# Optimization experiments

Hardware: AMD Instinct MI355X
Metric: run time of the kernel (lower is better)

## Reference

```python
import jax, jax.numpy as jnp
import numpy as np

NUM_HEADS = 16


def setup_inputs() -> dict:
    key = jax.random.key(0)
    k1, k2, k3, k4 = jax.random.split(key, 4)
    B, N, C = 4, 2048, 1024
    x = jax.random.normal(k1, (B, N, C), dtype=jnp.float32)
    # xavier-uniform-ish scaling for stable softmax
    Wqkv = jax.random.normal(k2, (C, 3 * C), dtype=jnp.float32) * (2.0 / (C + 3 * C)) ** 0.5
    Wproj = jax.random.normal(k3, (C, C), dtype=jnp.float32) * (1.0 / C) ** 0.5
    bproj = jnp.zeros((C,), dtype=jnp.float32)
    mask = jax.random.randint(k4, (B, N), 0, 2, dtype=jnp.int32)  # >0 means masked
    return {"x": x, "Wqkv": Wqkv, "Wproj": Wproj, "bproj": bproj, "mask": mask}


def reference(x, Wqkv, Wproj, bproj, mask):
    B, N, C = x.shape
    H = NUM_HEADS
    Dh = C // H
    scale = Dh ** -0.5
    qkv = x @ Wqkv                                   # [B, N, 3C]
    qkv = qkv.reshape(B, N, 3, H, Dh).transpose(2, 0, 3, 1, 4)  # [3, B, H, N, Dh]
    q, k, v = qkv[0], qkv[1], qkv[2]
    att = jnp.einsum('bhqd,bhkd->bhqk', q, k) * scale  # [B, H, N, N]
    att = jnp.where(mask[:, None, None, :] > 0, jnp.float32(-10000000.0), att)
    att = jax.nn.softmax(att, axis=-1)
    out = jnp.einsum('bhqk,bhkd->bhqd', att, v)      # [B, H, N, Dh]
    out = out.transpose(0, 2, 1, 3).reshape(B, N, C)
    return out @ Wproj + bproj
```

## Files before the change

kernel.cpp:

```cpp
#include <hip/hip_runtime.h>
#include <hip/hip_bf16.h>
#include <cstdint>

typedef __bf16 bf16x8 __attribute__((ext_vector_type(8)));
typedef float f32x4 __attribute__((ext_vector_type(4)));
typedef uint4 __attribute__((may_alias)) uint4a;

typedef __attribute__((address_space(3))) unsigned int   lds_u32;
typedef __attribute__((address_space(1))) const unsigned int gbl_u32;

#define BATCH 4
#define SEQ   2048
#define CDIM  1024
#define NH    16
#define HD    64
#define MROWS (BATCH*SEQ)

__device__ __forceinline__ unsigned short f2bf(float f) {
    uint32_t u = __builtin_bit_cast(uint32_t, f);
    u += 0x7fffu + ((u >> 16) & 1u);
    return (unsigned short)(u >> 16);
}

__device__ __forceinline__ void g2l16(const unsigned short* g, unsigned short* l) {
    __builtin_amdgcn_global_load_lds((gbl_u32*)g, (lds_u32*)l, 16, 0, 0);
}

__global__ void cvt_bf16_kernel(const float* __restrict__ in,
                                unsigned short* __restrict__ out, int n) {
    int i = (blockIdx.x * blockDim.x + threadIdx.x) * 4;
    if (i + 3 < n) {
        float4 v = *(const float4*)(in + i);
        ushort4 o;
        o.x = f2bf(v.x); o.y = f2bf(v.y); o.z = f2bf(v.z); o.w = f2bf(v.w);
        *(ushort4*)(out + i) = o;
    }
}

__global__ void transpose_cvt_kernel(const float* __restrict__ in,
                                     unsigned short* __restrict__ out,
                                     int R, int Cc) {
    __shared__ float tile[32][33];
    int c0 = blockIdx.x * 32, r0 = blockIdx.y * 32;
    int tx = threadIdx.x, ty = threadIdx.y;
    #pragma unroll
    for (int i = 0; i < 32; i += 8)
        tile[ty + i][tx] = in[(size_t)(r0 + ty + i) * Cc + c0 + tx];
    __syncthreads();
    #pragma unroll
    for (int i = 0; i < 32; i += 8)
        out[(size_t)(c0 + ty + i) * R + r0 + tx] = f2bf(tile[tx][ty + i]);
}

__global__ void mask_scan_kernel(const int* __restrict__ mask,
                                 int* __restrict__ pfx, int* __restrict__ cnt) {
    __shared__ int s[256];
    int b = blockIdx.x, t = threadIdx.x;
    int keep[8], lc = 0;
    #pragma unroll
    for (int u = 0; u < 8; ++u) {
        keep[u] = (mask[b * SEQ + t * 8 + u] > 0) ? 0 : 1;
        lc += keep[u];
    }
    s[t] = lc;
    __syncthreads();
    for (int d = 1; d < 256; d <<= 1) {
        int w = (t >= d) ? s[t - d] : 0;
        __syncthreads();
        s[t] += w;
        __syncthreads();
    }
    int pos = s[t] - lc;
    #pragma unroll
    for (int u = 0; u < 8; ++u) {
        int idx = b * SEQ + t * 8 + u;
        pfx[idx] = keep[u] ? pos++ : -1;
    }
    if (t == 255) cnt[b] = s[255];
}

#define BK 64

__global__ __launch_bounds__(256, 2)
void gemm_qkv_kernel(const unsigned short* __restrict__ A,
                     const unsigned short* __restrict__ Bt,
                     const int* __restrict__ pfx,
                     unsigned short* __restrict__ Q,
                     unsigned short* __restrict__ Kc,
                     unsigned short* __restrict__ Vct) {
    __shared__ __align__(16) unsigned short sA[128 * 64];
    __shared__ __align__(16) unsigned short sB[128 * 64];
    const int Kdim = 1024;
    int m0 = blockIdx.x * 128;
    int n0 = blockIdx.y * 128;
    int tid = threadIdx.x;
    int wave = tid >> 6, lane = tid & 63;
    int wm = (wave >> 1) * 64, wn = (wave & 1) * 64;
    int l15 = lane & 15, quad = lane >> 4;
    int lr = lane >> 3, lc8 = ((lane & 7) ^ lr) * 8;

    f32x4 acc[4][4] = {};

    for (int k0 = 0; k0 < Kdim; k0 += BK) {
        #pragma unroll
        for (int it = 0; it < 4; ++it) {
            int c = wave * 4 + it;
            int gr = c * 8 + lr;
            g2l16(A  + (size_t)(m0 + gr) * Kdim + k0 + lc8, &sA[c * 512]);
            g2l16(Bt + (size_t)(n0 + gr) * Kdim + k0 + lc8, &sB[c * 512]);
        }
        __syncthreads();
        #pragma unroll
        for (int kk = 0; kk < BK; kk += 32) {
            bf16x8 af[4], bfr[4];
            #pragma unroll
            for (int i = 0; i < 4; ++i) {
                int r = wm + i * 16 + l15;
                int q = ((kk >> 3) + quad) ^ (r & 7);
                af[i] = __builtin_bit_cast(bf16x8, *(const uint4a*)(&sA[r * 64 + q * 8]));
            }
            #pragma unroll
            for (int j = 0; j < 4; ++j) {
                int r = wn + j * 16 + l15;
                int q = ((kk >> 3) + quad) ^ (r & 7);
                bfr[j] = __builtin_bit_cast(bf16x8, *(const uint4a*)(&sB[r * 64 + q * 8]));
            }
            #pragma unroll
            for (int i = 0; i < 4; ++i)
                #pragma unroll
                for (int j = 0; j < 4; ++j)
                    acc[i][j] = __builtin_amdgcn_mfma_f32_16x16x32_bf16(af[i], bfr[j], acc[i][j], 0, 0, 0);
        }
        __syncthreads();
    }

    #pragma unroll
    for (int i = 0; i < 4; ++i) {
        #pragma unroll
        for (int j = 0; j < 4; ++j) {
            int col = n0 + wn + j * 16 + l15;
            int three = col >> 10;
            int h = (col >> 6) & 15;
            int d = col & 63;
            int row0 = m0 + wm + i * 16 + quad * 4;
            int b = row0 >> 11, n = row0 & 2047;
            size_t bh = (size_t)(b * NH + h);
            if (three == 0) {
                #pragma unroll
                for (int r = 0; r < 4; ++r)
                    Q[(bh * SEQ + n + r) * HD + d] = f2bf(acc[i][j][r]);
            } else if (three == 1) {
                #pragma unroll
                for (int r = 0; r < 4; ++r) {
                    int pf = pfx[(b << 11) + n + r];
                    if (pf >= 0) Kc[(bh * SEQ + pf) * HD + d] = f2bf(acc[i][j][r]);
                }
            } else {
                #pragma unroll
                for (int r = 0; r < 4; ++r) {
                    int pf = pfx[(b << 11) + n + r];
                    if (pf >= 0) Vct[(bh * HD + d) * SEQ + pf] = f2bf(acc[i][j][r]);
                }
            }
        }
    }
}

__global__ __launch_bounds__(256, 2)
void gemm_proj_kernel(const unsigned short* __restrict__ A,
                      const unsigned short* __restrict__ Bt,
                      const float* __restrict__ bias,
                      float* __restrict__ Out) {
    __shared__ __align__(16) unsigned short sA[128 * 64];
    __shared__ __align__(16) unsigned short sB[128 * 64];
    const int Kdim = 1024;
    int m0 = blockIdx.x * 128;
    int n0 = blockIdx.y * 128;
    int tid = threadIdx.x;
    int wave = tid >> 6, lane = tid & 63;
    int wm = (wave >> 1) * 64, wn = (wave & 1) * 64;
    int l15 = lane & 15, quad = lane >> 4;
    int lr = lane >> 3, lc8 = ((lane & 7) ^ lr) * 8;

    f32x4 acc[4][4] = {};

    for (int k0 = 0; k0 < Kdim; k0 += BK) {
        #pragma unroll
        for (int it = 0; it < 4; ++it) {
            int c = wave * 4 + it;
            int gr = c * 8 + lr;
            g2l16(A  + (size_t)(m0 + gr) * Kdim + k0 + lc8, &sA[c * 512]);
            g2l16(Bt + (size_t)(n0 + gr) * Kdim + k0 + lc8, &sB[c * 512]);
        }
        __syncthreads();
        #pragma unroll
        for (int kk = 0; kk < BK; kk += 32) {
            bf16x8 af[4], bfr[4];
            #pragma unroll
            for (int i = 0; i < 4; ++i) {
                int r = wm + i * 16 + l15;
                int q = ((kk >> 3) + quad) ^ (r & 7);
                af[i] = __builtin_bit_cast(bf16x8, *(const uint4a*)(&sA[r * 64 + q * 8]));
            }
            #pragma unroll
            for (int j = 0; j < 4; ++j) {
                int r = wn + j * 16 + l15;
                int q = ((kk >> 3) + quad) ^ (r & 7);
                bfr[j] = __builtin_bit_cast(bf16x8, *(const uint4a*)(&sB[r * 64 + q * 8]));
            }
            #pragma unroll
            for (int i = 0; i < 4; ++i)
                #pragma unroll
                for (int j = 0; j < 4; ++j)
                    acc[i][j] = __builtin_amdgcn_mfma_f32_16x16x32_bf16(af[i], bfr[j], acc[i][j], 0, 0, 0);
        }
        __syncthreads();
    }

    #pragma unroll
    for (int i = 0; i < 4; ++i) {
        #pragma unroll
        for (int j = 0; j < 4; ++j) {
            int col = n0 + wn + j * 16 + l15;
            float bv = bias[col];
            #pragma unroll
            for (int r = 0; r < 4; ++r) {
                int row = m0 + wm + i * 16 + quad * 4 + r;
                Out[(size_t)row * CDIM + col] = acc[i][j][r] + bv;
            }
        }
    }
}

#define SPD 72

__global__ __launch_bounds__(256, 4)
void flash_attn_kernel(const unsigned short* __restrict__ Q,
                       const unsigned short* __restrict__ Kg,
                       const unsigned short* __restrict__ Vt,
                       const int* __restrict__ cnt,
                       unsigned short* __restrict__ O) {
    int q0 = blockIdx.x * 128;
    int bh = blockIdx.y;
    int b = bh >> 4, h = bh & 15;
    int tid = threadIdx.x;
    int wave = tid >> 6, lane = tid & 63;
    int l15 = lane & 15, quad = lane >> 4;
    int lr = lane >> 3, lc8 = ((lane & 7) ^ lr) * 8;

    const int kn = cnt[b];

    const size_t head_off = (size_t)bh * SEQ * HD;
    const unsigned short* Qh = Q + head_off;
    const unsigned short* Kh = Kg + head_off;
    const unsigned short* Vh = Vt + head_off;

    __shared__ __align__(16) unsigned short sK [64 * 64];
    __shared__ __align__(16) unsigned short sVt[64 * 64];
    __shared__ __align__(16) unsigned short sP [4][2][16 * SPD];

    bf16x8 qf[2][2];
    #pragma unroll
    for (int mt = 0; mt < 2; ++mt) {
        const unsigned short* qp = Qh + (size_t)(q0 + wave * 32 + mt * 16 + l15) * HD + quad * 8;
        qf[mt][0] = __builtin_bit_cast(bf16x8, *(const uint4a*)(qp));
        qf[mt][1] = __builtin_bit_cast(bf16x8, *(const uint4a*)(qp + 32));
    }

    f32x4 oacc[2][4] = {};
    float lpart[2][4] = {};

    const float C1 = 0.18033688011112042f;

    for (int k0 = 0; k0 < kn; k0 += 64) {
        #pragma unroll
        for (int it = 0; it < 2; ++it) {
            int c = wave * 2 + it;
            int gr = c * 8 + lr;
            g2l16(Kh + (size_t)(k0 + gr) * HD + lc8, &sK[c * 512]);
            g2l16(Vh + (size_t)gr * SEQ + k0 + lc8, &sVt[c * 512]);
        }
        __syncthreads();

        float madd[4];
        #pragma unroll
        for (int j = 0; j < 4; ++j)
            madd[j] = (k0 + j * 16 + l15 < kn) ? 0.f : -1e30f;

        #pragma unroll
        for (int mt = 0; mt < 2; ++mt) {
            f32x4 s[4] = {};
            #pragma unroll
            for (int j = 0; j < 4; ++j) {
                int r = j * 16 + l15, sw = r & 7;
                uint4 v0 = *(const uint4a*)(&sK[r * 64 + ((quad ^ sw) * 8)]);
                uint4 v1 = *(const uint4a*)(&sK[r * 64 + (((4 + quad) ^ sw) * 8)]);
                s[j] = __builtin_amdgcn_mfma_f32_16x16x32_bf16(qf[mt][0], __builtin_bit_cast(bf16x8, v0), s[j], 0, 0, 0);
                s[j] = __builtin_amdgcn_mfma_f32_16x16x32_bf16(qf[mt][1], __builtin_bit_cast(bf16x8, v1), s[j], 0, 0, 0);
            }
            #pragma unroll
            for (int j = 0; j < 4; ++j)
                #pragma unroll
                for (int r = 0; r < 4; ++r) {
                    float p = __builtin_amdgcn_exp2f(fmaf(s[j][r], C1, madd[j]));
                    s[j][r] = p;
                    lpart[mt][r] += p;
                }
            unsigned short* sp = &sP[wave][mt][0];
            #pragma unroll
            for (int j = 0; j < 4; ++j)
                #pragma unroll
                for (int r = 0; r < 4; ++r)
                    sp[(quad * 4 + r) * SPD + j * 16 + l15] = f2bf(s[j][r]);
            #pragma unroll
            for (int kc = 0; kc < 2; ++kc) {
                uint4 av = *(const uint4a*)(&sp[l15 * SPD + kc * 32 + quad * 8]);
                bf16x8 af = __builtin_bit_cast(bf16x8, av);
                #pragma unroll
                for (int jd = 0; jd < 4; ++jd) {
                    int r = jd * 16 + l15;
                    int q = ((kc * 4 + quad) ^ (r & 7)) * 8;
                    uint4 bv = *(const uint4a*)(&sVt[r * 64 + q]);
                    oacc[mt][jd] = __builtin_amdgcn_mfma_f32_16x16x32_bf16(af, __builtin_bit_cast(bf16x8, bv), oacc[mt][jd], 0, 0, 0);
                }
            }
        }
        __syncthreads();
    }

    #pragma unroll
    for (int mt = 0; mt < 2; ++mt)
        #pragma unroll
        for (int r = 0; r < 4; ++r) {
            float v = lpart[mt][r];
            #pragma unroll
            for (int d = 1; d < 16; d <<= 1) v += __shfl_xor(v, d);
            lpart[mt][r] = v;
        }

    #pragma unroll
    for (int mt = 0; mt < 2; ++mt)
        #pragma unroll
        for (int jd = 0; jd < 4; ++jd) {
            int d = jd * 16 + l15;
            #pragma unroll
            for (int r = 0; r < 4; ++r) {
                int qrow = q0 + wave * 32 + mt * 16 + quad * 4 + r;
                float val = oacc[mt][jd][r] / lpart[mt][r];
                O[((size_t)(b * SEQ + qrow)) * CDIM + h * HD + d] = f2bf(val);
            }
        }
}

extern "C" void kernel_launch(void* const* d_in, const int* in_sizes, int n_in,
                              void* d_out, int out_size, void* d_ws, size_t ws_size,
                              hipStream_t stream) {
    const float* x     = (const float*)d_in[0];
    const float* Wqkv  = (const float*)d_in[1];
    const float* Wproj = (const float*)d_in[2];
    const float* bproj = (const float*)d_in[3];
    const int*   mask  = (const int*)d_in[4];
    float* out = (float*)d_out;

    char* ws = (char*)d_ws;
    unsigned short* xb     = (unsigned short*)(ws);
    unsigned short* Wqkvt  = (unsigned short*)(ws + (16u << 20));
    unsigned short* Wprojt = (unsigned short*)(ws + (22u << 20));
    unsigned short* Qb     = (unsigned short*)(ws + (24u << 20));
    unsigned short* Kb     = (unsigned short*)(ws + (40u << 20));
    unsigned short* Vtb    = (unsigned short*)(ws + (56u << 20));
    int*            pfx    = (int*)(ws + (72u << 20));
    int*            cntb   = (int*)(ws + (72u << 20) + (32u << 10));

    cvt_bf16_kernel<<<dim3(8192), dim3(256), 0, stream>>>(x, xb, MROWS * CDIM);
    transpose_cvt_kernel<<<dim3(96, 32), dim3(32, 8), 0, stream>>>(Wqkv, Wqkvt, 1024, 3072);
    transpose_cvt_kernel<<<dim3(32, 32), dim3(32, 8), 0, stream>>>(Wproj, Wprojt, 1024, 1024);
    mask_scan_kernel<<<dim3(4), dim3(256), 0, stream>>>(mask, pfx, cntb);
    gemm_qkv_kernel<<<dim3(64, 24), dim3(256), 0, stream>>>(xb, Wqkvt, pfx, Qb, Kb, Vtb);
    flash_attn_kernel<<<dim3(16, 64), dim3(256), 0, stream>>>(Qb, Kb, Vtb, cntb, xb);
    gemm_proj_kernel<<<dim3(64, 8), dim3(256), 0, stream>>>(xb, Wprojt, bproj, out);
}
```

Baseline: 256.0 us.

## Use packed bf16 conversion, shrink P scratch, raise attention occupancy, reorder grid

Replaces scalar float-to-bf16 rounding with the packed hardware conversion builtin wherever bf16 is produced (input cast, Q store, P tile, attention output). The P staging buffer in shared memory drops to one tile per wave, and launch bounds rise to six blocks per CU. The attention grid is swapped so consecutive blocks cover different heads for the same query tile, and the softmax divide becomes a reciprocal-multiply. This targets ALU cost and occupancy. The risks are register spilling under the tighter bound and small rounding differences from the approximate reciprocal.

```diff
diff --git a/kernel.cpp b/kernel.cpp
--- a/kernel.cpp
+++ b/kernel.cpp
@@ -22,6 +22,18 @@
     return (unsigned short)(u >> 16);
 }
 
+#if __has_builtin(__builtin_amdgcn_cvt_pk_bf16_f32)
+typedef __bf16 bf16x2 __attribute__((ext_vector_type(2)));
+__device__ __forceinline__ uint32_t pk2bf(float a, float b) {
+    bf16x2 v = __builtin_amdgcn_cvt_pk_bf16_f32(a, b);
+    return __builtin_bit_cast(uint32_t, v);
+}
+#else
+__device__ __forceinline__ uint32_t pk2bf(float a, float b) {
+    return (uint32_t)f2bf(a) | ((uint32_t)f2bf(b) << 16);
+}
+#endif
+
 __device__ __forceinline__ void g2l16(const unsigned short* g, unsigned short* l) {
     __builtin_amdgcn_global_load_lds((gbl_u32*)g, (lds_u32*)l, 16, 0, 0);
 }
@@ -31,9 +43,10 @@
     int i = (blockIdx.x * blockDim.x + threadIdx.x) * 4;
     if (i + 3 < n) {
         float4 v = *(const float4*)(in + i);
-        ushort4 o;
-        o.x = f2bf(v.x); o.y = f2bf(v.y); o.z = f2bf(v.z); o.w = f2bf(v.w);
-        *(ushort4*)(out + i) = o;
+        uint2 o;
+        o.x = pk2bf(v.x, v.y);
+        o.y = pk2bf(v.z, v.w);
+        *(uint2*)(out + i) = o;
     }
 }
 
@@ -146,9 +159,13 @@
             int b = row0 >> 11, n = row0 & 2047;
             size_t bh = (size_t)(b * NH + h);
             if (three == 0) {
-                #pragma unroll
-                for (int r = 0; r < 4; ++r)
-                    Q[(bh * SEQ + n + r) * HD + d] = f2bf(acc[i][j][r]);
+                uint32_t p01 = pk2bf(acc[i][j][0], acc[i][j][1]);
+                uint32_t p23 = pk2bf(acc[i][j][2], acc[i][j][3]);
+                size_t base = (bh * SEQ + n) * HD + d;
+                Q[base]          = (unsigned short)p01;
+                Q[base + HD]     = (unsigned short)(p01 >> 16);
+                Q[base + 2 * HD] = (unsigned short)p23;
+                Q[base + 3 * HD] = (unsigned short)(p23 >> 16);
             } else if (three == 1) {
                 #pragma unroll
                 for (int r = 0; r < 4; ++r) {
@@ -234,14 +251,14 @@
 
 #define SPD 72
 
-__global__ __launch_bounds__(256, 4)
+__global__ __launch_bounds__(256, 6)
 void flash_attn_kernel(const unsigned short* __restrict__ Q,
                        const unsigned short* __restrict__ Kg,
                        const unsigned short* __restrict__ Vt,
                        const int* __restrict__ cnt,
                        unsigned short* __restrict__ O) {
-    int q0 = blockIdx.x * 128;
-    int bh = blockIdx.y;
+    int bh = blockIdx.x;
+    int q0 = blockIdx.y * 128;
     int b = bh >> 4, h = bh & 15;
     int tid = threadIdx.x;
     int wave = tid >> 6, lane = tid & 63;
@@ -257,7 +274,7 @@
 
     __shared__ __align__(16) unsigned short sK [64 * 64];
     __shared__ __align__(16) unsigned short sVt[64 * 64];
-    __shared__ __align__(16) unsigned short sP [4][2][16 * SPD];
+    __shared__ __align__(16) unsigned short sP [4][16 * SPD];
 
     bf16x8 qf[2][2];
     #pragma unroll
@@ -298,20 +315,23 @@
                 s[j] = __builtin_amdgcn_mfma_f32_16x16x32_bf16(qf[mt][0], __builtin_bit_cast(bf16x8, v0), s[j], 0, 0, 0);
                 s[j] = __builtin_amdgcn_mfma_f32_16x16x32_bf16(qf[mt][1], __builtin_bit_cast(bf16x8, v1), s[j], 0, 0, 0);
             }
-            #pragma unroll
-            for (int j = 0; j < 4; ++j)
+            unsigned short* sp = &sP[wave][0];
+            #pragma unroll
+            for (int j = 0; j < 4; ++j) {
                 #pragma unroll
                 for (int r = 0; r < 4; ++r) {
                     float p = __builtin_amdgcn_exp2f(fmaf(s[j][r], C1, madd[j]));
                     s[j][r] = p;
                     lpart[mt][r] += p;
                 }
-            unsigned short* sp = &sP[wave][mt][0];
-            #pragma unroll
-            for (int j = 0; j < 4; ++j)
-                #pragma unroll
-                for (int r = 0; r < 4; ++r)
-                    sp[(quad * 4 + r) * SPD + j * 16 + l15] = f2bf(s[j][r]);
+                uint32_t p01 = pk2bf(s[j][0], s[j][1]);
+                uint32_t p23 = pk2bf(s[j][2], s[j][3]);
+                int base = quad * 4 * SPD + j * 16 + l15;
+                sp[base]           = (unsigned short)p01;
+                sp[base + SPD]     = (unsigned short)(p01 >> 16);
+                sp[base + 2 * SPD] = (unsigned short)p23;
+                sp[base + 3 * SPD] = (unsigned short)(p23 >> 16);
+            }
             #pragma unroll
             for (int kc = 0; kc < 2; ++kc) {
                 uint4 av = *(const uint4a*)(&sp[l15 * SPD + kc * 32 + quad * 8]);
@@ -328,6 +348,7 @@
         __syncthreads();
     }
 
+    float rl[2][4];
     #pragma unroll
     for (int mt = 0; mt < 2; ++mt)
         #pragma unroll
@@ -335,7 +356,7 @@
             float v = lpart[mt][r];
             #pragma unroll
             for (int d = 1; d < 16; d <<= 1) v += __shfl_xor(v, d);
-            lpart[mt][r] = v;
+            rl[mt][r] = __builtin_amdgcn_rcpf(v);
         }
 
     #pragma unroll
@@ -343,12 +364,13 @@
         #pragma unroll
         for (int jd = 0; jd < 4; ++jd) {
             int d = jd * 16 + l15;
-            #pragma unroll
-            for (int r = 0; r < 4; ++r) {
-                int qrow = q0 + wave * 32 + mt * 16 + quad * 4 + r;
-                float val = oacc[mt][jd][r] / lpart[mt][r];
-                O[((size_t)(b * SEQ + qrow)) * CDIM + h * HD + d] = f2bf(val);
-            }
+            size_t base = ((size_t)(b * SEQ + q0 + wave * 32 + mt * 16 + quad * 4)) * CDIM + h * HD + d;
+            uint32_t p01 = pk2bf(oacc[mt][jd][0] * rl[mt][0], oacc[mt][jd][1] * rl[mt][1]);
+            uint32_t p23 = pk2bf(oacc[mt][jd][2] * rl[mt][2], oacc[mt][jd][3] * rl[mt][3]);
+            O[base]            = (unsigned short)p01;
+            O[base + CDIM]     = (unsigned short)(p01 >> 16);
+            O[base + 2 * CDIM] = (unsigned short)p23;
+            O[base + 3 * CDIM] = (unsigned short)(p23 >> 16);
         }
 }
 
@@ -377,6 +399,6 @@
     transpose_cvt_kernel<<<dim3(32, 32), dim3(32, 8), 0, stream>>>(Wproj, Wprojt, 1024, 1024);
     mask_scan_kernel<<<dim3(4), dim3(256), 0, stream>>>(mask, pfx, cntb);
     gemm_qkv_kernel<<<dim3(64, 24), dim3(256), 0, stream>>>(xb, Wqkvt, pfx, Qb, Kb, Vtb);
-    flash_attn_kernel<<<dim3(16, 64), dim3(256), 0, stream>>>(Qb, Kb, Vtb, cntb, xb);
+    flash_attn_kernel<<<dim3(64, 16), dim3(256), 0, stream>>>(Qb, Kb, Vtb, cntb, xb);
     gemm_proj_kernel<<<dim3(64, 8), dim3(256), 0, stream>>>(xb, Wprojt, bproj, out);
 }
```

After: 299.2 us. 1.17x slower.
